# Kernel tuning notes

Measured on AMD Instinct MI355X. Metric: run time of the kernel, lower is better.

The kernel has to match this reference:

```python
import jax, jax.numpy as jnp
import numpy as np

B, IN, OUT, M = 4096, 512, 512, 16


def setup_inputs() -> dict:
    key = jax.random.key(0)
    k1, k2, k3 = jax.random.split(key, 3)
    # inputs kept strictly positive and inside the physical range [0, 60]
    x = jax.random.uniform(k1, (B, IN), jnp.float32, 0.1, 10.0)
    # photonic basis coefficients: positive, with small polynomial terms
    b_coef = jax.random.uniform(k2, (M, 8), jnp.float32, 0.1, 0.9)
    b_coef = b_coef.at[:, 4:].multiply(0.01)
    coeffs = 0.01 * jax.random.normal(k3, (OUT, IN, M), jnp.float32)
    return {"x": x, "coeffs": coeffs, "b_coef": b_coef}


def _photonic_basis(x, b):
    # x: (B, IN) -> broadcast against M basis functions -> (B, IN, M)
    xe = x[:, :, None]                                   # (B, IN, 1)
    b1, b2, b3, b4, b5, b6, b7, b8 = [b[:, i][None, None, :] for i in range(8)]
    inner = jnp.expm1(b3 * xe)
    powered = jnp.power(inner, b4)
    y = (b1 * jnp.log(1.0 + b2 * jnp.log1p(powered))
         + b5 * xe + b6 * xe**2 + b7 * xe**3 + b8 * xe**4)
    return y


def reference(x, coeffs, b_coef):
    # basis: (B, IN, M); double reduce over (IN, M) == GEMM of size B x (IN*M) x OUT
    basis = _photonic_basis(x, b_coef)
    y = jnp.einsum('bim,oim->bo', basis, coeffs)         # (B, OUT)
    return y
```

## Files before the change

kernel.cpp:

```cpp
#include <hip/hip_runtime.h>
#include <hip/hip_bf16.h>
#include <stdint.h>

#define B_DIM   4096
#define IN_DIM  512
#define OUT_DIM 512
#define M_DIM   16
#define K_DIM   (IN_DIM * M_DIM)
#define MN      (B_DIM * OUT_DIM)

typedef unsigned short ushort_t;
typedef __attribute__((ext_vector_type(8))) __bf16 bf16x8;
typedef __attribute__((ext_vector_type(4))) float  f32x4;

__device__ __forceinline__ ushort_t f2bf(float f) {
  union { float f; uint32_t u; } v; v.f = f;
  uint32_t u = v.u + 0x7fffu + ((v.u >> 16) & 1u);
  return (ushort_t)(u >> 16);
}

__global__ __launch_bounds__(256) void convert_coeffs_kernel(
    const float* __restrict__ src, ushort_t* __restrict__ dst, int n4) {
  int i = blockIdx.x * 256 + threadIdx.x;
  if (i >= n4) return;
  float4 v = ((const float4*)src)[i];
  ushort4 o;
  o.x = f2bf(v.x); o.y = f2bf(v.y); o.z = f2bf(v.z); o.w = f2bf(v.w);
  ((ushort4*)dst)[i] = o;
}

__global__ __launch_bounds__(256) void basis_kernel(
    const float* __restrict__ x, const float* __restrict__ bc,
    ushort_t* __restrict__ basis) {
  int idx = blockIdx.x * 256 + threadIdx.x;
  float xv = x[idx];
  float x2 = xv * xv, x3 = x2 * xv, x4 = x2 * x2;
  const float LOG2E = 1.44269504088896340736f;
  const float LN2   = 0.69314718055994530942f;
  uint32_t w[8];
  #pragma unroll
  for (int m = 0; m < 16; ++m) {
    float b1 = bc[m*8+0], b2 = bc[m*8+1], b3 = bc[m*8+2], b4 = bc[m*8+3];
    float b5 = bc[m*8+4], b6 = bc[m*8+5], b7 = bc[m*8+6], b8 = bc[m*8+7];
    float e     = __builtin_amdgcn_exp2f(b3 * xv * LOG2E);
    float inner = e - 1.0f;
    float p     = __builtin_amdgcn_exp2f(b4 * __builtin_amdgcn_logf(inner));
    float u     = LN2 * __builtin_amdgcn_logf(1.0f + p);
    float vv    = LN2 * __builtin_amdgcn_logf(1.0f + b2 * u);
    float y = b1 * vv + b5 * xv + b6 * x2 + b7 * x3 + b8 * x4;
    uint32_t h = (uint32_t)f2bf(y);
    if (m & 1) w[m >> 1] |= (h << 16); else w[m >> 1] = h;
  }
  uint4* dst = (uint4*)(basis + (size_t)idx * 16);
  dst[0] = make_uint4(w[0], w[1], w[2], w[3]);
  dst[1] = make_uint4(w[4], w[5], w[6], w[7]);
}

#define BM 128
#define BN 128
#define BK 32
#define SPLITK 4
#define KC (K_DIM / SPLITK)

#define GLD16(g, l) \
  __builtin_amdgcn_global_load_lds((const __attribute__((address_space(1))) void*)(g), \
                                   (__attribute__((address_space(3))) void*)(l), 16, 0, 0)

template <int ATOMIC>
__global__ __launch_bounds__(256, 2) void gemm_kernel(
    const ushort_t* __restrict__ A,
    const ushort_t* __restrict__ Bt,
    float* __restrict__ P) {
  __shared__ __align__(16) ushort_t As[BM * BK];
  __shared__ __align__(16) ushort_t Bs[BN * BK];
  const int tid  = threadIdx.x;
  const int wave = tid >> 6;
  const int lane = tid & 63;
  const int bm = blockIdx.x, bn = blockIdx.y, ks = blockIdx.z;

  const int srow = wave * 16 + (lane >> 2);
  const int scol = (lane & 3) * 8;
  const ushort_t* Ag  = A  + (size_t)(bm * BM + srow) * K_DIM + (size_t)ks * KC + scol;
  const ushort_t* Bg  = Bt + (size_t)(bn * BN + srow) * K_DIM + (size_t)ks * KC + scol;
  const ushort_t* Ag2 = Ag + (size_t)64 * K_DIM;
  const ushort_t* Bg2 = Bg + (size_t)64 * K_DIM;
  ushort_t* AsW  = As + wave * 16 * BK;
  ushort_t* AsW2 = AsW + 64 * BK;
  ushort_t* BsW  = Bs + wave * 16 * BK;
  ushort_t* BsW2 = BsW + 64 * BK;

  const int wr = wave >> 1, wc = wave & 1;
  const int fm = lane & 15;
  const int fk = (lane >> 4) * 8;

  f32x4 acc[4][4] = {};

  for (int kt = 0; kt < KC; kt += BK) {
    GLD16(Ag, AsW); GLD16(Ag2, AsW2);
    GLD16(Bg, BsW); GLD16(Bg2, BsW2);
    Ag += BK; Ag2 += BK; Bg += BK; Bg2 += BK;
    __syncthreads();
    bf16x8 af[4], bfv[4];
    #pragma unroll
    for (int t = 0; t < 4; ++t) {
      af[t]  = *(const bf16x8*)(As + (wr * 64 + t * 16 + fm) * BK + fk);
      bfv[t] = *(const bf16x8*)(Bs + (wc * 64 + t * 16 + fm) * BK + fk);
    }
    #pragma unroll
    for (int mt = 0; mt < 4; ++mt)
      #pragma unroll
      for (int nt = 0; nt < 4; ++nt)
        acc[mt][nt] = __builtin_amdgcn_mfma_f32_16x16x32_bf16(af[mt], bfv[nt], acc[mt][nt], 0, 0, 0);
    __syncthreads();
  }

  const int colb = bn * BN + wc * 64 + fm;
  const int rowb = bm * BM + wr * 64 + (lane >> 4) * 4;
  float* out = P + (ATOMIC ? (size_t)0 : (size_t)ks * MN);
  #pragma unroll
  for (int mt = 0; mt < 4; ++mt) {
    #pragma unroll
    for (int nt = 0; nt < 4; ++nt) {
      #pragma unroll
      for (int j = 0; j < 4; ++j) {
        int row = rowb + mt * 16 + j;
        int col = colb + nt * 16;
        float vv = acc[mt][nt][j];
        if (ATOMIC) atomicAdd(out + (size_t)row * OUT_DIM + col, vv);
        else        out[(size_t)row * OUT_DIM + col] = vv;
      }
    }
  }
}

__global__ __launch_bounds__(256) void reduce_kernel(
    const float* __restrict__ P, float* __restrict__ out) {
  int i = blockIdx.x * 256 + threadIdx.x;
  const float4* p = (const float4*)P;
  float4 a = p[i], b = p[i + MN/4], c = p[i + 2*(MN/4)], d = p[i + 3*(MN/4)];
  float4 r = make_float4(a.x + b.x + c.x + d.x, a.y + b.y + c.y + d.y,
                         a.z + b.z + c.z + d.z, a.w + b.w + c.w + d.w);
  ((float4*)out)[i] = r;
}

extern "C" void kernel_launch(void* const* d_in, const int* in_sizes, int n_in,
                              void* d_out, int out_size, void* d_ws, size_t ws_size,
                              hipStream_t stream) {
  const float* x      = (const float*)d_in[0];
  const float* coeffs = (const float*)d_in[1];
  const float* b_coef = (const float*)d_in[2];
  float* out = (float*)d_out;
  char*  ws  = (char*)d_ws;

  const size_t BASIS_BYTES = (size_t)B_DIM * K_DIM * 2;
  const size_t COEF_BYTES  = (size_t)OUT_DIM * K_DIM * 2;
  ushort_t* basis = (ushort_t*)ws;
  ushort_t* coefb = (ushort_t*)(ws + BASIS_BYTES);
  float* partials = (float*)(ws + BASIS_BYTES + COEF_BYTES);
  const size_t FULL = BASIS_BYTES + COEF_BYTES + (size_t)SPLITK * MN * 4;
  const bool use_atomic = (ws_size < FULL);

  convert_coeffs_kernel<<<(OUT_DIM * K_DIM / 4 + 255) / 256, 256, 0, stream>>>(
      coeffs, coefb, OUT_DIM * K_DIM / 4);
  basis_kernel<<<(B_DIM * IN_DIM) / 256, 256, 0, stream>>>(x, b_coef, basis);

  dim3 grid(B_DIM / BM, OUT_DIM / BN, SPLITK);
  if (use_atomic) {
    hipMemsetAsync(d_out, 0, (size_t)MN * 4, stream);
    gemm_kernel<1><<<grid, 256, 0, stream>>>(basis, coefb, out);
  } else {
    gemm_kernel<0><<<grid, 256, 0, stream>>>(basis, coefb, partials);
    reduce_kernel<<<MN / 4 / 256, 256, 0, stream>>>(partials, out);
  }
}
```

Measured before the change: 148.9 us.

## Double-buffer GEMM LDS, swizzle layout, raise split-K, merge prep kernels

Adds double-buffered LDS staging to the bf16 MFMA GEMM so global-to-LDS loads for the next tile overlap compute on the current one. It also XOR-swizzles the LDS column layout to reduce bank conflicts, doubles split-K from 4 to 8 with an occupancy hint of 4, and fuses the coefficient-conversion and basis kernels into one launch. The cost is double the LDS per block and twice the partial-sum traffic in the reduce step.

Measured after the change: 147.7 us. About the same (-0.8%).

```diff
diff --git a/kernel.cpp b/kernel.cpp
--- a/kernel.cpp
+++ b/kernel.cpp
@@ -19,20 +19,25 @@
   return (ushort_t)(u >> 16);
 }
 
-__global__ __launch_bounds__(256) void convert_coeffs_kernel(
-    const float* __restrict__ src, ushort_t* __restrict__ dst, int n4) {
-  int i = blockIdx.x * 256 + threadIdx.x;
-  if (i >= n4) return;
-  float4 v = ((const float4*)src)[i];
-  ushort4 o;
-  o.x = f2bf(v.x); o.y = f2bf(v.y); o.z = f2bf(v.z); o.w = f2bf(v.w);
-  ((ushort4*)dst)[i] = o;
-}
+#define CONV_N4      (OUT_DIM * K_DIM / 4)
+#define CONV_BLOCKS  (CONV_N4 / 256)
+#define BASIS_BLOCKS (B_DIM * IN_DIM / 256)
 
-__global__ __launch_bounds__(256) void basis_kernel(
+__global__ __launch_bounds__(256) void prep_kernel(
+    const float* __restrict__ coeffs, ushort_t* __restrict__ coefb,
     const float* __restrict__ x, const float* __restrict__ bc,
     ushort_t* __restrict__ basis) {
-  int idx = blockIdx.x * 256 + threadIdx.x;
+  const int blk = blockIdx.x;
+  const int tid = threadIdx.x;
+  if (blk < CONV_BLOCKS) {
+    int i = blk * 256 + tid;
+    float4 v = ((const float4*)coeffs)[i];
+    ushort4 o;
+    o.x = f2bf(v.x); o.y = f2bf(v.y); o.z = f2bf(v.z); o.w = f2bf(v.w);
+    ((ushort4*)coefb)[i] = o;
+    return;
+  }
+  int idx = (blk - CONV_BLOCKS) * 256 + tid;
   float xv = x[idx];
   float x2 = xv * xv, x3 = x2 * xv, x4 = x2 * x2;
   const float LOG2E = 1.44269504088896340736f;
@@ -59,60 +64,74 @@
 #define BM 128
 #define BN 128
 #define BK 32
-#define SPLITK 4
+#define SPLITK 8
 #define KC (K_DIM / SPLITK)
+#define NITER (KC / BK)
 
 #define GLD16(g, l) \
   __builtin_amdgcn_global_load_lds((const __attribute__((address_space(1))) void*)(g), \
                                    (__attribute__((address_space(3))) void*)(l), 16, 0, 0)
 
 template <int ATOMIC>
-__global__ __launch_bounds__(256, 2) void gemm_kernel(
+__global__ __launch_bounds__(256, 4) void gemm_kernel(
     const ushort_t* __restrict__ A,
     const ushort_t* __restrict__ Bt,
     float* __restrict__ P) {
-  __shared__ __align__(16) ushort_t As[BM * BK];
-  __shared__ __align__(16) ushort_t Bs[BN * BK];
+  __shared__ __align__(16) ushort_t As[2][BM * BK];
+  __shared__ __align__(16) ushort_t Bs[2][BN * BK];
   const int tid  = threadIdx.x;
   const int wave = tid >> 6;
   const int lane = tid & 63;
   const int bm = blockIdx.x, bn = blockIdx.y, ks = blockIdx.z;
 
   const int srow = wave * 16 + (lane >> 2);
-  const int scol = (lane & 3) * 8;
+  const int scol = (((lane & 3) ^ ((lane >> 3) & 3)) * 8);
   const ushort_t* Ag  = A  + (size_t)(bm * BM + srow) * K_DIM + (size_t)ks * KC + scol;
   const ushort_t* Bg  = Bt + (size_t)(bn * BN + srow) * K_DIM + (size_t)ks * KC + scol;
   const ushort_t* Ag2 = Ag + (size_t)64 * K_DIM;
   const ushort_t* Bg2 = Bg + (size_t)64 * K_DIM;
-  ushort_t* AsW  = As + wave * 16 * BK;
-  ushort_t* AsW2 = AsW + 64 * BK;
-  ushort_t* BsW  = Bs + wave * 16 * BK;
-  ushort_t* BsW2 = BsW + 64 * BK;
+  const int lofs  = wave * 16 * BK;
+  const int lofs2 = (wave * 16 + 64) * BK;
+
+#define STAGE(b) do { \
+    GLD16(Ag,  &As[b][lofs]);  GLD16(Ag2, &As[b][lofs2]); \
+    GLD16(Bg,  &Bs[b][lofs]);  GLD16(Bg2, &Bs[b][lofs2]); \
+    Ag += BK; Ag2 += BK; Bg += BK; Bg2 += BK; } while (0)
 
   const int wr = wave >> 1, wc = wave & 1;
   const int fm = lane & 15;
-  const int fk = (lane >> 4) * 8;
+  const int fkswz = (((lane >> 4) ^ ((lane >> 1) & 3)) << 3);
 
   f32x4 acc[4][4] = {};
 
-  for (int kt = 0; kt < KC; kt += BK) {
-    GLD16(Ag, AsW); GLD16(Ag2, AsW2);
-    GLD16(Bg, BsW); GLD16(Bg2, BsW2);
-    Ag += BK; Ag2 += BK; Bg += BK; Bg2 += BK;
+#define COMPUTE(b) do { \
+    bf16x8 af[4], bfv[4]; \
+    _Pragma("unroll") \
+    for (int t = 0; t < 4; ++t) { \
+      af[t]  = *(const bf16x8*)&As[b][(wr * 64 + t * 16 + fm) * BK + fkswz]; \
+      bfv[t] = *(const bf16x8*)&Bs[b][(wc * 64 + t * 16 + fm) * BK + fkswz]; \
+    } \
+    _Pragma("unroll") \
+    for (int mt = 0; mt < 4; ++mt) \
+      _Pragma("unroll") \
+      for (int nt = 0; nt < 4; ++nt) \
+        acc[mt][nt] = __builtin_amdgcn_mfma_f32_16x16x32_bf16(af[mt], bfv[nt], acc[mt][nt], 0, 0, 0); \
+  } while (0)
+
+  STAGE(0);
+  for (int kt = 0; kt < NITER - 2; kt += 2) {
     __syncthreads();
-    bf16x8 af[4], bfv[4];
-    #pragma unroll
-    for (int t = 0; t < 4; ++t) {
-      af[t]  = *(const bf16x8*)(As + (wr * 64 + t * 16 + fm) * BK + fk);
-      bfv[t] = *(const bf16x8*)(Bs + (wc * 64 + t * 16 + fm) * BK + fk);
-    }
-    #pragma unroll
-    for (int mt = 0; mt < 4; ++mt)
-      #pragma unroll
-      for (int nt = 0; nt < 4; ++nt)
-        acc[mt][nt] = __builtin_amdgcn_mfma_f32_16x16x32_bf16(af[mt], bfv[nt], acc[mt][nt], 0, 0, 0);
+    STAGE(1);
+    COMPUTE(0);
     __syncthreads();
+    STAGE(0);
+    COMPUTE(1);
   }
+  __syncthreads();
+  STAGE(1);
+  COMPUTE(0);
+  __syncthreads();
+  COMPUTE(1);
 
   const int colb = bn * BN + wc * 64 + fm;
   const int rowb = bm * BM + wr * 64 + (lane >> 4) * 4;
@@ -131,15 +150,20 @@
       }
     }
   }
+#undef STAGE
+#undef COMPUTE
 }
 
 __global__ __launch_bounds__(256) void reduce_kernel(
     const float* __restrict__ P, float* __restrict__ out) {
   int i = blockIdx.x * 256 + threadIdx.x;
   const float4* p = (const float4*)P;
-  float4 a = p[i], b = p[i + MN/4], c = p[i + 2*(MN/4)], d = p[i + 3*(MN/4)];
-  float4 r = make_float4(a.x + b.x + c.x + d.x, a.y + b.y + c.y + d.y,
-                         a.z + b.z + c.z + d.z, a.w + b.w + c.w + d.w);
+  float4 r = p[i];
+  #pragma unroll
+  for (int s = 1; s < SPLITK; ++s) {
+    float4 v = p[i + (size_t)s * (MN / 4)];
+    r.x += v.x; r.y += v.y; r.z += v.z; r.w += v.w;
+  }
   ((float4*)out)[i] = r;
 }
 
@@ -160,9 +184,8 @@
   const size_t FULL = BASIS_BYTES + COEF_BYTES + (size_t)SPLITK * MN * 4;
   const bool use_atomic = (ws_size < FULL);
 
-  convert_coeffs_kernel<<<(OUT_DIM * K_DIM / 4 + 255) / 256, 256, 0, stream>>>(
-      coeffs, coefb, OUT_DIM * K_DIM / 4);
-  basis_kernel<<<(B_DIM * IN_DIM) / 256, 256, 0, stream>>>(x, b_coef, basis);
+  prep_kernel<<<CONV_BLOCKS + BASIS_BLOCKS, 256, 0, stream>>>(
+      coeffs, coefb, x, b_coef, basis);
 
   dim3 grid(B_DIM / BM, OUT_DIM / BN, SPLITK);
   if (use_atomic) {
```
